# Performance work log

Measured on AMD Instinct MI355X. Metric: run time of the kernel, lower is better.

## Reference

```python
import jax, jax.numpy as jnp
import numpy as np

# BERT-base geometry
B, N, H, DH = 4, 512, 12, 64
HID = H * DH            # 768
E = 65536               # total edges (~avg degree 32)
NREL = 64               # relation vocabulary


def setup_inputs() -> dict:
    key = jax.random.key(0)
    ks = jax.random.split(key, 12)
    node_states = jax.random.normal(ks[0], (B, N, HID), jnp.float32)
    b = jax.random.randint(ks[1], (E,), 0, B)
    hn = jax.random.randint(ks[2], (E,), 0, N)
    tn = jax.random.randint(ks[3], (E,), 0, N)
    r = jax.random.randint(ks[4], (E,), 0, NREL)
    edge_indices = jnp.stack([b, hn, tn, r]).astype(jnp.int32)  # (4, E)
    node_type_ids = jnp.zeros((B, N), jnp.int32)  # unused by this subclass
    sc = 0.02
    Wq = jax.random.normal(ks[5], (HID, HID), jnp.float32) * sc
    bq = jnp.zeros((HID,), jnp.float32)
    Wk = jax.random.normal(ks[6], (HID, HID), jnp.float32) * sc
    bk = jnp.zeros((HID,), jnp.float32)
    Wv = jax.random.normal(ks[7], (HID, HID), jnp.float32) * sc
    bv = jnp.zeros((HID,), jnp.float32)
    # relation matrix embeddings: one (DH, DH) matrix per relation id
    rel_emb = jnp.eye(DH, dtype=jnp.float32)[None] + jax.random.normal(ks[8], (NREL, DH, DH), jnp.float32) * sc
    return {"node_states": node_states, "edge_indices": edge_indices,
            "node_type_ids": node_type_ids, "Wq": Wq, "bq": bq,
            "Wk": Wk, "bk": bk, "Wv": Wv, "bv": bv, "rel_emb": rel_emb}


def reference(node_states, edge_indices, node_type_ids, Wq, bq, Wk, bk, Wv, bv, rel_emb):
    Bq, Nn, hid = node_states.shape
    # dense QKV projections (torch Linear: y = x @ W^T + b)
    Q = node_states @ Wq.T + bq
    K = node_states @ Wk.T + bk
    V = (node_states @ Wv.T + bv).reshape(Bq, Nn, H, DH)  # (B,N,H,D)
    be, he, te, re = edge_indices  # each (E,)
    # per-edge gathers
    Qe = Q[be, he].reshape(-1, H, DH)   # (E,H,D)
    Ke = K[be, te].reshape(-1, H, DH)   # (E,H,D)
    Re = rel_emb[re]                     # (E,D,D) relation matrix per edge
    # Q projected through relation matrix, then inner product with K per head
    Qp = jnp.einsum('ehd,edk->ehk', Qe, Re)
    logits = jnp.einsum('ehd,ehd->eh', Qp, Ke) / jnp.sqrt(jnp.float32(DH))  # (E,H)
    # sparse softmax over tail nodes: segment = (batch, head_node)
    seg = be * Nn + he
    nseg = Bq * Nn
    m = jax.ops.segment_max(logits, seg, num_segments=nseg)      # (BN,H)
    ex = jnp.exp(logits - m[seg])
    denom = jax.ops.segment_sum(ex, seg, num_segments=nseg)      # (BN,H)
    p = ex / denom[seg]                                          # (E,H)
    # dropout prob = 0.0 (deterministic reference)
    # aggregate: out[b,i,h,:] = sum_edges p_e * V[b, tail_e, h, :]
    contrib = p[:, :, None] * V[be, te]                          # (E,H,D)
    out = jax.ops.segment_sum(contrib, seg, num_segments=nseg)   # (BN,H,D)
    return out.reshape(Bq, Nn, H * DH)
```

## Files before the change

### kernel.cpp

```cpp
#include <hip/hip_runtime.h>
#include <hip/hip_bf16.h>

#define NB   4
#define NN   512
#define NH   12
#define DHD  64
#define HID  768
#define NE   65536
#define NSEG 2048
#define NREL 64
#define LGS  16
#define SCAP 128
#define NSUB2 8
#define RSUB (NREL * NSUB2)
#define RCAP 256
#define RLY2 12
#define POISON 0xAAAAAAAAu

typedef short bf16x8 __attribute__((ext_vector_type(8)));
typedef float f32x4  __attribute__((ext_vector_type(4)));
typedef unsigned short u16x8 __attribute__((ext_vector_type(8)));

__device__ __forceinline__ unsigned short f2bf(float f) {
    __hip_bfloat16 h = __float2bfloat16(f);
    return *reinterpret_cast<unsigned short*>(&h);
}
__device__ __forceinline__ float bf2f(unsigned short s) {
    return __int_as_float(((int)s) << 16);
}
__device__ __forceinline__ int unpz(int v) {
    return (int)((unsigned)v - POISON);
}

#define NQKV 576
__global__ __launch_bounds__(256) void qkv_scatter_kernel(
    const float* __restrict__ Xf,
    const float* __restrict__ Wq, const float* __restrict__ Wk,
    const float* __restrict__ Wv,
    const float* __restrict__ bq, const float* __restrict__ bk,
    const float* __restrict__ bv,
    unsigned short* __restrict__ Qh, unsigned short* __restrict__ Kh,
    unsigned short* __restrict__ Vh,
    const int* __restrict__ ei,
    int* __restrict__ cursor, int* __restrict__ rcursor,
    int* __restrict__ s_te, int* __restrict__ s_pkr)
{
    __shared__ __align__(16) char smem[64 * 132 * 4];
    const int tid = threadIdx.x;

    if (blockIdx.x >= NQKV) {
        const int e = (blockIdx.x - NQKV) * 256 + tid;
        const int b  = ei[e];
        const int hn = ei[NE + e];
        const int tn = ei[2 * NE + e];
        const int rr = ei[3 * NE + e];
        const int seg = b * NN + hn;
        const int slot = unpz(atomicAdd(&cursor[seg], 1)) & (SCAP - 1);
        const int pos  = seg * SCAP + slot;
        s_te[pos] = tn;
        const int rsub = rr * NSUB2 + ((e >> 8) & (NSUB2 - 1));
        const int rj = unpz(atomicAdd(&rcursor[rsub], 1)) & (RCAP - 1);
        int2 pv2; pv2.x = (seg << 9) | tn; pv2.y = pos;
        ((int2*)s_pkr)[rsub * RCAP + rj] = pv2;
        return;
    }

    const int bid = blockIdx.x;
    const int z   = bid / 192;
    const int rem = bid - z * 192;
    const int by  = rem / 6;
    const int bx  = rem - by * 6;
    const float* Wf = (z == 0) ? Wq : ((z == 1) ? Wk : Wv);
    const float* bias = (z == 0) ? bq : ((z == 1) ? bk : bv);

    const int n0 = bx * 128;
    const int m0 = by * 64;
    const int lane = tid & 63;
    const int wave = tid >> 6;
    const int wm = wave >> 1, wn = wave & 1;

    unsigned short* As = (unsigned short*)smem;
    unsigned short* Bs = (unsigned short*)(smem + 8192);
    float* Cs = (float*)smem;

    f32x4 acc[2][4];
    #pragma unroll
    for (int a = 0; a < 2; ++a)
        #pragma unroll
        for (int b2 = 0; b2 < 4; ++b2) acc[a][b2] = (f32x4){0.f, 0.f, 0.f, 0.f};

    const int ml = lane & 15;
    const int q4 = lane >> 4;

    for (int k0 = 0; k0 < HID; k0 += 64) {
        __syncthreads();
        #pragma unroll
        for (int i = 0; i < 2; ++i) {
            const int idx = i * 256 + tid;
            const int row = idx >> 3;
            const int kq  = (idx & 7) ^ (row & 7);
            const float* s4 = Xf + (size_t)(m0 + row) * HID + k0 + kq * 8;
            const float4 va = ((const float4*)s4)[0];
            const float4 vb = ((const float4*)s4)[1];
            u16x8 r8;
            r8[0] = f2bf(va.x); r8[1] = f2bf(va.y);
            r8[2] = f2bf(va.z); r8[3] = f2bf(va.w);
            r8[4] = f2bf(vb.x); r8[5] = f2bf(vb.y);
            r8[6] = f2bf(vb.z); r8[7] = f2bf(vb.w);
            *(u16x8*)(As + idx * 8) = r8;
        }
        #pragma unroll
        for (int i = 0; i < 4; ++i) {
            const int idx = i * 256 + tid;
            const int row = idx >> 3;
            const int kq  = (idx & 7) ^ (row & 7);
            const float* s4 = Wf + (size_t)(n0 + row) * HID + k0 + kq * 8;
            const float4 va = ((const float4*)s4)[0];
            const float4 vb = ((const float4*)s4)[1];
            u16x8 r8;
            r8[0] = f2bf(va.x); r8[1] = f2bf(va.y);
            r8[2] = f2bf(va.z); r8[3] = f2bf(va.w);
            r8[4] = f2bf(vb.x); r8[5] = f2bf(vb.y);
            r8[6] = f2bf(vb.z); r8[7] = f2bf(vb.w);
            *(u16x8*)(Bs + idx * 8) = r8;
        }
        __syncthreads();

        #pragma unroll
        for (int ks = 0; ks < 2; ++ks) {
            bf16x8 af[2], bfr[4];
            #pragma unroll
            for (int t = 0; t < 2; ++t) {
                const int ar = wm * 32 + t * 16 + ml;
                const int ac = (ks * 4 + q4) ^ (ar & 7);
                af[t] = *(const bf16x8*)(As + ar * 64 + ac * 8);
            }
            #pragma unroll
            for (int t = 0; t < 4; ++t) {
                const int br = wn * 64 + t * 16 + ml;
                const int bc = (ks * 4 + q4) ^ (br & 7);
                bfr[t] = *(const bf16x8*)(Bs + br * 64 + bc * 8);
            }
            #pragma unroll
            for (int mt = 0; mt < 2; ++mt)
                #pragma unroll
                for (int nt = 0; nt < 4; ++nt)
                    acc[mt][nt] = __builtin_amdgcn_mfma_f32_16x16x32_bf16(
                        af[mt], bfr[nt], acc[mt][nt], 0, 0, 0);
        }
    }

    __syncthreads();
    #pragma unroll
    for (int mt = 0; mt < 2; ++mt)
        #pragma unroll
        for (int nt = 0; nt < 4; ++nt)
            #pragma unroll
            for (int rg = 0; rg < 4; ++rg)
                Cs[(wm * 32 + mt * 16 + q4 * 4 + rg) * 132 +
                   wn * 64 + nt * 16 + ml] = acc[mt][nt][rg];
    __syncthreads();

    unsigned short* Y = (z == 0) ? Qh : ((z == 1) ? Kh : Vh);
    #pragma unroll
    for (int it = 0; it < 4; ++it) {
        const int id  = tid + it * 256;
        const int row = id >> 4;
        const int cg  = id & 15;
        const float* cp = Cs + row * 132 + cg * 8;
        const float4 cA = *(const float4*)cp;
        const float4 cB = *(const float4*)(cp + 4);
        const float* bp = bias + n0 + cg * 8;
        const float4 bA = *(const float4*)bp;
        const float4 bB = *(const float4*)(bp + 4);
        const size_t o = (size_t)(m0 + row) * HID + n0 + cg * 8;
        u16x8 r;
        r[0] = f2bf(cA.x + bA.x); r[1] = f2bf(cA.y + bA.y);
        r[2] = f2bf(cA.z + bA.z); r[3] = f2bf(cA.w + bA.w);
        r[4] = f2bf(cB.x + bB.x); r[5] = f2bf(cB.y + bB.y);
        r[6] = f2bf(cB.z + bB.z); r[7] = f2bf(cB.w + bB.w);
        *(u16x8*)&Y[o] = r;
    }
}

__global__ __launch_bounds__(256) void rel_logits(
    const unsigned short* __restrict__ Qh, const unsigned short* __restrict__ Kh,
    const float* __restrict__ rel,
    const int* __restrict__ rcursor, const int* __restrict__ s_pkr,
    float* __restrict__ Lg)
{
    const int rs = blockIdx.x;
    int cnt = unpz(rcursor[rs]);
    cnt = (cnt < 0) ? 0 : ((cnt > RCAP) ? RCAP : cnt);
    const int rows = cnt * NH;
    if ((int)blockIdx.y * 256 >= rows) return;
    const int r = rs >> 3;
    const int tid = threadIdx.x;
    const int lane = tid & 63;
    const int wave = tid >> 6;

    __shared__ int qb[256], kb[256], oi[256];
    __shared__ float QpS[4][16][68];

    bf16x8 bfrag[2][4];
    {
        const float* Rg = rel + (size_t)r * 4096;
        const int q4 = lane >> 4, n = lane & 15;
        #pragma unroll
        for (int ks = 0; ks < 2; ++ks)
            #pragma unroll
            for (int nt = 0; nt < 4; ++nt) {
                bf16x8 f;
                #pragma unroll
                for (int j = 0; j < 8; ++j)
                    f[j] = (short)f2bf(Rg[(ks * 32 + q4 * 8 + j) * 64 + nt * 16 + n]);
                bfrag[ks][nt] = f;
            }
    }

    for (int t0 = blockIdx.y * 256; t0 < rows; t0 += RLY2 * 256) {
        __syncthreads();
        {
            const int rowid = t0 + tid;
            if (rowid < rows) {
                const int el = rowid / 12;
                const int h  = rowid - el * 12;
                const int2 v = ((const int2*)s_pkr)[rs * RCAP + el];
                const int pos = v.y & (NSEG * SCAP - 1);
                const int sg  = (v.x >> 9) & (NSEG - 1);
                const int te  = v.x & (NN - 1);
                qb[tid] = sg * HID + h * 64;
                kb[tid] = ((sg & ~(NN - 1)) + te) * HID + h * 64;
                oi[tid] = pos * LGS + h;
            } else { qb[tid] = 0; kb[tid] = 0; oi[tid] = -1; }
        }
        __syncthreads();

        for (int g = wave; g < 16; g += 4) {
            const int m = lane & 15, q4 = lane >> 4;
            const int qbase = qb[g * 16 + m];
            f32x4 cfr[4] = {{0,0,0,0},{0,0,0,0},{0,0,0,0},{0,0,0,0}};
            #pragma unroll
            for (int ks = 0; ks < 2; ++ks) {
                const bf16x8 afr = *(const bf16x8*)(Qh + qbase + ks * 32 + q4 * 8);
                #pragma unroll
                for (int nt = 0; nt < 4; ++nt)
                    cfr[nt] = __builtin_amdgcn_mfma_f32_16x16x32_bf16(
                        afr, bfrag[ks][nt], cfr[nt], 0, 0, 0);
            }
            #pragma unroll
            for (int nt = 0; nt < 4; ++nt)
                #pragma unroll
                for (int rg = 0; rg < 4; ++rg)
                    QpS[wave][q4 * 4 + rg][nt * 16 + m] = cfr[nt][rg];

            const int rw = lane >> 2, ch = (lane & 3) * 16;
            const int rowid2 = g * 16 + rw;
            const int kbase = kb[rowid2];
            const bf16x8 k0 = *(const bf16x8*)(Kh + kbase + ch);
            const bf16x8 k1 = *(const bf16x8*)(Kh + kbase + ch + 8);
            float s = 0.f;
            #pragma unroll
            for (int i = 0; i < 8; ++i) {
                s = fmaf(QpS[wave][rw][ch + i],     bf2f((unsigned short)k0[i]), s);
                s = fmaf(QpS[wave][rw][ch + 8 + i], bf2f((unsigned short)k1[i]), s);
            }
            s += __shfl_xor(s, 1, 64);
            s += __shfl_xor(s, 2, 64);
            if ((lane & 3) == 0) {
                const int o = oi[rowid2];
                if (o >= 0) Lg[o] = __expf(s * 0.125f);
            }
        }
    }
}

__global__ __launch_bounds__(256) void seg_softmax_agg(
    const unsigned short* __restrict__ Vh, const float* __restrict__ Lg,
    const int* __restrict__ s_te,
    float* __restrict__ out,
    int* __restrict__ cursor, int* __restrict__ rcursor)
{
    const int seg  = blockIdx.x;
    const int tid  = threadIdx.x;
    int cnt = unpz(cursor[seg]);
    __syncthreads();
    if (tid == 0) {
        cursor[seg] = (int)POISON;
        if (seg < RSUB) rcursor[seg] = (int)POISON;
    }
    cnt = (cnt < 0) ? 0 : ((cnt > SCAP) ? SCAP : cnt);
    const int base = seg * SCAP;
    const int lane = tid & 63;
    const int w    = tid >> 6;
    const int browbase = seg & ~(NN - 1);

    __shared__ int   te_s[64];
    __shared__ float pv[4][3][64];

    float l0 = 0.f, l1 = 0.f, l2 = 0.f;
    float acc0 = 0.f, acc1 = 0.f, acc2 = 0.f;

    for (int c0 = 0; c0 < cnt; c0 += 64) {
        const int cc = min(64, cnt - c0);
        __syncthreads();
        if (tid < cc) te_s[tid] = s_te[base + c0 + tid] & (NN - 1);
        __syncthreads();

        float p0 = 0.f, p1 = 0.f, p2 = 0.f;
        if (lane < cc) {
            const float* Lp = Lg + (size_t)(base + c0 + lane) * LGS;
            p0 = Lp[w]; p1 = Lp[4 + w]; p2 = Lp[8 + w];
        }
        float s0 = p0, s1 = p1, s2 = p2;
        #pragma unroll
        for (int o = 1; o < 64; o <<= 1) {
            s0 += __shfl_xor(s0, o, 64);
            s1 += __shfl_xor(s1, o, 64);
            s2 += __shfl_xor(s2, o, 64);
        }
        l0 += s0; l1 += s1; l2 += s2;
        pv[w][0][lane] = p0; pv[w][1][lane] = p1; pv[w][2][lane] = p2;

        for (int j = 0; j < cc; ++j) {
            const unsigned short* __restrict__ Vr =
                Vh + (size_t)(browbase + te_s[j]) * HID + lane;
            acc0 = fmaf(pv[w][0][j], bf2f(Vr[w * 64]),       acc0);
            acc1 = fmaf(pv[w][1][j], bf2f(Vr[(4 + w) * 64]), acc1);
            acc2 = fmaf(pv[w][2][j], bf2f(Vr[(8 + w) * 64]), acc2);
        }
    }

    float* Yo = out + (size_t)seg * HID;
    Yo[tid]       = (l0 > 0.f) ? acc0 / l0 : 0.f;
    Yo[tid + 256] = (l1 > 0.f) ? acc1 / l1 : 0.f;
    Yo[tid + 512] = (l2 > 0.f) ? acc2 / l2 : 0.f;
}

extern "C" void kernel_launch(void* const* d_in, const int* in_sizes, int n_in,
                              void* d_out, int out_size, void* d_ws, size_t ws_size,
                              hipStream_t stream)
{
    const float* X   = (const float*)d_in[0];
    const int*   EI  = (const int*)d_in[1];
    const float* Wq  = (const float*)d_in[3];
    const float* bq  = (const float*)d_in[4];
    const float* Wk  = (const float*)d_in[5];
    const float* bk  = (const float*)d_in[6];
    const float* Wv  = (const float*)d_in[7];
    const float* bv  = (const float*)d_in[8];
    const float* rel = (const float*)d_in[9];
    float* out = (float*)d_out;

    char* p = (char*)d_ws;
    unsigned short* Qh = (unsigned short*)p;  p += (size_t)NSEG * HID * 2;
    unsigned short* Kh = (unsigned short*)p;  p += (size_t)NSEG * HID * 2;
    unsigned short* Vh = (unsigned short*)p;  p += (size_t)NSEG * HID * 2;
    float* Lg = (float*)p;                    p += (size_t)NSEG * SCAP * LGS * 4;
    int* cursor   = (int*)p;                  p += NSEG * 4;
    int* rcursor  = (int*)p;                  p += RSUB * 4;
    int* s_te     = (int*)p;                  p += (size_t)NSEG * SCAP * 4;
    int* s_pkr    = (int*)p;                  p += (size_t)RSUB * RCAP * 8;

    qkv_scatter_kernel<<<NQKV + 256, 256, 0, stream>>>(
        X, Wq, Wk, Wv, bq, bk, bv, Qh, Kh, Vh,
        EI, cursor, rcursor, s_te, s_pkr);
    rel_logits<<<dim3(RSUB, RLY2), 256, 0, stream>>>(
        Qh, Kh, rel, rcursor, s_pkr, Lg);
    seg_softmax_agg<<<NSEG, 256, 0, stream>>>(
        Vh, Lg, s_te, out, cursor, rcursor);
}
```

Measured before the change: 187.4 us.

## Prefetch next GEMM K-tile into registers and stage relation fragments via LDS

The QKV GEMM now loads the next K-slice of X and W from global memory into registers while the current slice is being computed, and it hoists address math out of the loop. This overlaps global-load latency with the MFMA work, at the cost of more registers. Launch bounds are raised to request 4 blocks per SM. In rel_logits, each block now reads the relation matrix with coalesced float4 loads into shared memory in fragment order, then reads its bf16 fragments from there, replacing strided scalar global reads per lane.

Result: faster. 170.3 us (-9.1%).

```diff
diff --git a/kernel.cpp b/kernel.cpp
--- a/kernel.cpp
+++ b/kernel.cpp
@@ -33,7 +33,7 @@
 }
 
 #define NQKV 576
-__global__ __launch_bounds__(256) void qkv_scatter_kernel(
+__global__ __launch_bounds__(256, 4) void qkv_scatter_kernel(
     const float* __restrict__ Xf,
     const float* __restrict__ Wq, const float* __restrict__ Wk,
     const float* __restrict__ Wv,
@@ -92,37 +92,64 @@
     const int ml = lane & 15;
     const int q4 = lane >> 4;
 
+    int offA[2], offB[4];
+    #pragma unroll
+    for (int i = 0; i < 2; ++i) {
+        const int idx = i * 256 + tid;
+        const int row = idx >> 3;
+        const int kq  = (idx & 7) ^ (row & 7);
+        offA[i] = (m0 + row) * HID + kq * 8;
+    }
+    #pragma unroll
+    for (int i = 0; i < 4; ++i) {
+        const int idx = i * 256 + tid;
+        const int row = idx >> 3;
+        const int kq  = (idx & 7) ^ (row & 7);
+        offB[i] = (n0 + row) * HID + kq * 8;
+    }
+
+    float4 a0[2], a1[2], b0[4], b1[4];
+    #pragma unroll
+    for (int i = 0; i < 2; ++i) {
+        const float4* s = (const float4*)(Xf + offA[i]);
+        a0[i] = s[0]; a1[i] = s[1];
+    }
+    #pragma unroll
+    for (int i = 0; i < 4; ++i) {
+        const float4* s = (const float4*)(Wf + offB[i]);
+        b0[i] = s[0]; b1[i] = s[1];
+    }
+
     for (int k0 = 0; k0 < HID; k0 += 64) {
-        __syncthreads();
         #pragma unroll
         for (int i = 0; i < 2; ++i) {
-            const int idx = i * 256 + tid;
-            const int row = idx >> 3;
-            const int kq  = (idx & 7) ^ (row & 7);
-            const float* s4 = Xf + (size_t)(m0 + row) * HID + k0 + kq * 8;
-            const float4 va = ((const float4*)s4)[0];
-            const float4 vb = ((const float4*)s4)[1];
             u16x8 r8;
-            r8[0] = f2bf(va.x); r8[1] = f2bf(va.y);
-            r8[2] = f2bf(va.z); r8[3] = f2bf(va.w);
-            r8[4] = f2bf(vb.x); r8[5] = f2bf(vb.y);
-            r8[6] = f2bf(vb.z); r8[7] = f2bf(vb.w);
-            *(u16x8*)(As + idx * 8) = r8;
+            r8[0] = f2bf(a0[i].x); r8[1] = f2bf(a0[i].y);
+            r8[2] = f2bf(a0[i].z); r8[3] = f2bf(a0[i].w);
+            r8[4] = f2bf(a1[i].x); r8[5] = f2bf(a1[i].y);
+            r8[6] = f2bf(a1[i].z); r8[7] = f2bf(a1[i].w);
+            *(u16x8*)(As + (i * 256 + tid) * 8) = r8;
         }
         #pragma unroll
         for (int i = 0; i < 4; ++i) {
-            const int idx = i * 256 + tid;
-            const int row = idx >> 3;
-            const int kq  = (idx & 7) ^ (row & 7);
-            const float* s4 = Wf + (size_t)(n0 + row) * HID + k0 + kq * 8;
-            const float4 va = ((const float4*)s4)[0];
-            const float4 vb = ((const float4*)s4)[1];
             u16x8 r8;
-            r8[0] = f2bf(va.x); r8[1] = f2bf(va.y);
-            r8[2] = f2bf(va.z); r8[3] = f2bf(va.w);
-            r8[4] = f2bf(vb.x); r8[5] = f2bf(vb.y);
-            r8[6] = f2bf(vb.z); r8[7] = f2bf(vb.w);
-            *(u16x8*)(Bs + idx * 8) = r8;
+            r8[0] = f2bf(b0[i].x); r8[1] = f2bf(b0[i].y);
+            r8[2] = f2bf(b0[i].z); r8[3] = f2bf(b0[i].w);
+            r8[4] = f2bf(b1[i].x); r8[5] = f2bf(b1[i].y);
+            r8[6] = f2bf(b1[i].z); r8[7] = f2bf(b1[i].w);
+            *(u16x8*)(Bs + (i * 256 + tid) * 8) = r8;
+        }
+        if (k0 + 64 < HID) {
+            #pragma unroll
+            for (int i = 0; i < 2; ++i) {
+                const float4* s = (const float4*)(Xf + offA[i] + k0 + 64);
+                a0[i] = s[0]; a1[i] = s[1];
+            }
+            #pragma unroll
+            for (int i = 0; i < 4; ++i) {
+                const float4* s = (const float4*)(Wf + offB[i] + k0 + 64);
+                b0[i] = s[0]; b1[i] = s[1];
+            }
         }
         __syncthreads();
 
@@ -148,9 +175,9 @@
                     acc[mt][nt] = __builtin_amdgcn_mfma_f32_16x16x32_bf16(
                         af[mt], bfr[nt], acc[mt][nt], 0, 0, 0);
         }
-    }
-
-    __syncthreads();
+        __syncthreads();
+    }
+
     #pragma unroll
     for (int mt = 0; mt < 2; ++mt)
         #pragma unroll
@@ -201,22 +228,32 @@
 
     __shared__ int qb[256], kb[256], oi[256];
     __shared__ float QpS[4][16][68];
-
-    bf16x8 bfrag[2][4];
+    __shared__ __align__(16) unsigned short frS[4096];
+
     {
         const float* Rg = rel + (size_t)r * 4096;
-        const int q4 = lane >> 4, n = lane & 15;
-        #pragma unroll
-        for (int ks = 0; ks < 2; ++ks)
-            #pragma unroll
-            for (int nt = 0; nt < 4; ++nt) {
-                bf16x8 f;
-                #pragma unroll
-                for (int j = 0; j < 8; ++j)
-                    f[j] = (short)f2bf(Rg[(ks * 32 + q4 * 8 + j) * 64 + nt * 16 + n]);
-                bfrag[ks][nt] = f;
-            }
-    }
+        #pragma unroll
+        for (int it = 0; it < 4; ++it) {
+            const int i4 = it * 256 + tid;
+            const float4 v4 = ((const float4*)Rg)[i4];
+            const int d  = i4 >> 4;
+            const int c0 = (i4 & 15) * 4;
+            const int ks = d >> 5, q4 = (d >> 3) & 3, j = d & 7;
+            const float vv[4] = {v4.x, v4.y, v4.z, v4.w};
+            #pragma unroll
+            for (int e = 0; e < 4; ++e) {
+                const int c = c0 + e, nt = c >> 4, n = c & 15;
+                frS[((ks * 4 + nt) * 64 + q4 * 16 + n) * 8 + j] = f2bf(vv[e]);
+            }
+        }
+    }
+    __syncthreads();
+    bf16x8 bfrag[2][4];
+    #pragma unroll
+    for (int ks = 0; ks < 2; ++ks)
+        #pragma unroll
+        for (int nt = 0; nt < 4; ++nt)
+            bfrag[ks][nt] = *(const bf16x8*)(frS + ((ks * 4 + nt) * 64 + lane) * 8);
 
     for (int t0 = blockIdx.y * 256; t0 < rows; t0 += RLY2 * 256) {
         __syncthreads();
```
